# Performance work log

Hardware: AMD Instinct MI355X
Metric: run time of the kernel (lower is better)

The kernel has to match this reference:

```python
import jax, jax.numpy as jnp
import numpy as np

T, B, D, H = 1024, 128, 512, 256

def _linear_params(k, out_dim, in_dim):
    kw, kb = jax.random.split(k)
    s = 1.0 / np.sqrt(in_dim)
    w = jax.random.uniform(kw, (out_dim, in_dim), minval=-s, maxval=s, dtype=jnp.float32)
    b = jax.random.uniform(kb, (out_dim,), minval=-s, maxval=s, dtype=jnp.float32)
    return w, b

def setup_inputs() -> dict:
    key = jax.random.key(0)
    ks = jax.random.split(key, 9)
    x = jax.random.normal(ks[0], (T, B, D), dtype=jnp.float32)
    fc_w, fc_b = _linear_params(ks[1], H, D)
    forget_w, forget_b = _linear_params(ks[2], H, 2 * H)
    input_w, input_b = _linear_params(ks[3], H, 2 * H)
    update_w, update_b = _linear_params(ks[4], H, 2 * H)
    output_w, output_b = _linear_params(ks[5], H, 2 * H)
    cls_w0, cls_b0 = _linear_params(ks[6], H, H)
    cls_w1, cls_b1 = _linear_params(ks[7], H, H)
    cls_w2, cls_b2 = _linear_params(ks[8], 2, H)
    return dict(x=x, fc_w=fc_w, fc_b=fc_b,
                forget_w=forget_w, forget_b=forget_b,
                input_w=input_w, input_b=input_b,
                update_w=update_w, update_b=update_b,
                output_w=output_w, output_b=output_b,
                cls_w0=cls_w0, cls_b0=cls_b0,
                cls_w1=cls_w1, cls_b1=cls_b1,
                cls_w2=cls_w2, cls_b2=cls_b2)

def reference(x, fc_w, fc_b, forget_w, forget_b, input_w, input_b,
              update_w, update_b, output_w, output_b,
              cls_w0, cls_b0, cls_w1, cls_b1, cls_w2, cls_b2):
    # FC + tanh: [T,B,D] -> [T,B,H]
    h = jnp.tanh(x @ fc_w.T + fc_b)

    # LSTM-style gating over the leading time axis (state is [B,H])
    def step(carry, inp):
        hx, cx = carry
        comb = jnp.concatenate([inp, hx], axis=-1)  # [B, 2H]
        f = jax.nn.sigmoid(comb @ forget_w.T + forget_b)
        i = jax.nn.sigmoid(comb @ input_w.T + input_b)
        g = jnp.tanh(comb @ update_w.T + update_b)
        o = jax.nn.sigmoid(comb @ output_w.T + output_b)
        cx = f * cx + i * g
        hx = o * jnp.tanh(cx)
        return (hx, cx), hx

    init = (jnp.zeros((B, H), h.dtype), jnp.zeros((B, H), h.dtype))
    _, hs = jax.lax.scan(step, init, h)  # hs: [T,B,H]

    # classifier MLP (depth=2) -> 2 logits
    z = jax.nn.relu(hs @ cls_w0.T + cls_b0)
    z = jax.nn.relu(z @ cls_w1.T + cls_b1)
    return z @ cls_w2.T + cls_b2  # [T,B,2]
```

## Files before the change

kernel.cpp:

```cpp
#include <hip/hip_runtime.h>
#include <cstdint>

#define TT 1024
#define BB 128
#define DD 512
#define HH 256
#define TBR (TT*BB)

typedef __attribute__((ext_vector_type(8))) short  s8v;
typedef __attribute__((ext_vector_type(4))) float  f4v;
typedef __attribute__((ext_vector_type(4))) unsigned u4v;

__device__ __forceinline__ float sigf(float x) { return 1.0f / (1.0f + expf(-x)); }

__device__ __forceinline__ unsigned rnbf(float f) {
    unsigned u = __builtin_bit_cast(unsigned, f);
    return (u + 0x7FFFu + ((u >> 16) & 1u)) >> 16;
}

__global__ __launch_bounds__(256) void pack_kernel(
    const float* __restrict__ fw, const float* __restrict__ iw,
    const float* __restrict__ uw, const float* __restrict__ ow,
    const float* __restrict__ fb, const float* __restrict__ ib,
    const float* __restrict__ ub, const float* __restrict__ obb,
    float* __restrict__ wx_p, float* __restrict__ wh_p, float* __restrict__ b_p)
{
    const int r = blockIdx.x;
    const int gate = r >> 8, h = r & 255;
    const float* wsrc = gate == 0 ? fw : gate == 1 ? iw : gate == 2 ? uw : ow;
    const float* bsrc = gate == 0 ? fb : gate == 1 ? ib : gate == 2 ? ub : obb;
    const int k = threadIdx.x;
    wx_p[(size_t)r * 256 + k] = wsrc[(size_t)h * 512 + k];
    wh_p[(size_t)r * 256 + k] = wsrc[(size_t)h * 512 + 256 + k];
    if (k == 0) b_p[r] = bsrc[h];
}

__global__ __launch_bounds__(256) void pack_mfma(
    const float* __restrict__ fw, const float* __restrict__ iw,
    const float* __restrict__ uw, const float* __restrict__ ow,
    const float* __restrict__ fb, const float* __restrict__ ib,
    const float* __restrict__ ub, const float* __restrict__ obb,
    float* __restrict__ wx_p, float* __restrict__ wh_p, float* __restrict__ b_p)
{
    const int r = blockIdx.x;
    const int gate = (r >> 5) & 3;
    const int h = (r >> 7) * 32 + (r & 31);
    const float* wsrc = gate == 0 ? fw : gate == 1 ? iw : gate == 2 ? uw : ow;
    const float* bsrc = gate == 0 ? fb : gate == 1 ? ib : gate == 2 ? ub : obb;
    const int k = threadIdx.x;
    wx_p[(size_t)r * 256 + k] = wsrc[(size_t)h * 512 + k];
    wh_p[(size_t)r * 256 + k] = wsrc[(size_t)h * 512 + 256 + k];
    if (k == 0) b_p[r] = bsrc[h];
}

template<int K, int ACT, int PERM>
__global__ __launch_bounds__(256) void gemm_kernel(
    const float* A, const float* __restrict__ W,
    const float* __restrict__ bias, float* C, int N)
{
    __shared__ __align__(16) float As[16][192];
    __shared__ __align__(16) float Wt[16][192];
    const int tid = threadIdx.x;
    const int m0 = blockIdx.x * 128, n0 = blockIdx.y * 128;
    const int tm = tid >> 4, tn = tid & 15;
    const int am = tm * 12, wn = tn * 12;
    float acc[8][8] = {};
    for (int kc = 0; kc < K; kc += 16) {
        #pragma unroll
        for (int i = 0; i < 2; ++i) {
            int f4 = tid + 256 * i;
            int r = f4 >> 2, k4 = (f4 & 3) * 4;
            float4 av = *(const float4*)&A[(size_t)(m0 + r) * K + kc + k4];
            float4 wv = *(const float4*)&W[(size_t)(n0 + r) * K + kc + k4];
            int fo = (r >> 3) * 12 + (r & 7);
            As[k4 + 0][fo] = av.x; As[k4 + 1][fo] = av.y;
            As[k4 + 2][fo] = av.z; As[k4 + 3][fo] = av.w;
            Wt[k4 + 0][fo] = wv.x; Wt[k4 + 1][fo] = wv.y;
            Wt[k4 + 2][fo] = wv.z; Wt[k4 + 3][fo] = wv.w;
        }
        __syncthreads();
        #pragma unroll
        for (int kk = 0; kk < 16; ++kk) {
            float a[8], w[8];
            *(float4*)&a[0] = *(const float4*)&As[kk][am];
            *(float4*)&a[4] = *(const float4*)&As[kk][am + 4];
            *(float4*)&w[0] = *(const float4*)&Wt[kk][wn];
            *(float4*)&w[4] = *(const float4*)&Wt[kk][wn + 4];
            #pragma unroll
            for (int i = 0; i < 8; ++i)
                #pragma unroll
                for (int j = 0; j < 8; ++j)
                    acc[i][j] = fmaf(a[i], w[j], acc[i][j]);
        }
        __syncthreads();
    }
    #pragma unroll
    for (int i = 0; i < 8; ++i) {
        int m = m0 + tm * 8 + i;
        #pragma unroll
        for (int jh = 0; jh < 2; ++jh) {
            float4 v; float* vp = (float*)&v;
            #pragma unroll
            for (int l = 0; l < 4; ++l) {
                int n = n0 + tn * 8 + jh * 4 + l;
                float t = acc[i][jh * 4 + l] + bias[n];
                if (ACT == 1) t = tanhf(t);
                if (ACT == 2) t = fmaxf(t, 0.0f);
                vp[l] = t;
            }
            int nb = n0 + tn * 8 + jh * 4;
            int nc = PERM ? (((nb & 255) >> 3) * 32 + ((nb >> 8) << 3) + (nb & 7)) : nb;
            *(float4*)&C[(size_t)m * N + nc] = v;
        }
    }
}

__global__ __launch_bounds__(256, 1) void recur_mfma(
    float* __restrict__ h_buf,
    const float* __restrict__ xg,
    const float* __restrict__ wh_mf,
    unsigned* hxh, unsigned* hxl,
    int* flags)
{
    __shared__ __align__(16) unsigned ldsH[16 * 128];
    __shared__ __align__(16) unsigned ldsL[16 * 128];
    __shared__ float pre[16][132];
    const int tid = threadIdx.x;
    const int lane = tid & 63;
    const int wv = tid >> 6;
    const int bg = blockIdx.x & 7, hg = blockIdx.x >> 3;
    const int b0 = bg * 16;
    const int nlo = lane & 15, quad = lane >> 4;

    s8v bh[2][8], bl[2][8];
    #pragma unroll
    for (int nt = 0; nt < 2; ++nt) {
        int r = hg * 128 + wv * 32 + nt * 16 + nlo;
        #pragma unroll
        for (int ks = 0; ks < 8; ++ks) {
            const float* src = wh_mf + (size_t)r * 256 + ks * 32 + quad * 8;
            u4v uh, ul;
            #pragma unroll
            for (int p = 0; p < 4; ++p) {
                float f0 = src[2 * p], f1 = src[2 * p + 1];
                unsigned h0 = rnbf(f0), h1 = rnbf(f1);
                float r0 = f0 - __builtin_bit_cast(float, h0 << 16);
                float r1 = f1 - __builtin_bit_cast(float, h1 << 16);
                uh[p] = h0 | (rnbf(0.0f), h1 << 16);
                uh[p] = h0 | (h1 << 16);
                ul[p] = rnbf(r0) | (rnbf(r1) << 16);
            }
            bh[nt][ks] = __builtin_bit_cast(s8v, uh);
            bl[nt][ks] = __builtin_bit_cast(s8v, ul);
        }
    }

    const int sm = tid >> 4;
    const int sc0 = (tid & 15) * 2;
    const int cb = tid >> 4, q = tid & 15;

    float cx0 = 0.0f, cx1 = 0.0f;

    for (int t = 0; t < TT; ++t) {
        float2 xq[4];
        {
            const float* xr = xg + ((size_t)t * BB + b0 + cb) * 1024 + hg * 128 + 2 * q;
            #pragma unroll
            for (int g = 0; g < 4; ++g)
                xq[g] = *(const float2*)&xr[g * 32];
        }
        if (t > 0) {
            const int* fp = flags + ((size_t)(t - 1) * 8 + bg) * 8 + (lane & 7);
            long bud = 1L << 22;
            for (;;) {
                int v = __hip_atomic_load(fp, __ATOMIC_RELAXED, __HIP_MEMORY_SCOPE_AGENT);
                if (__all(v != 0)) break;
                if (--bud < 0) break;
                __builtin_amdgcn_s_sleep(1);
            }
        }
        {
            const size_t rowd = ((size_t)(t & 1) * 128 + b0 + sm) * 128 + sc0 * 4;
            const unsigned long long* gh = (const unsigned long long*)(hxh + rowd);
            const unsigned long long* gl = (const unsigned long long*)(hxl + rowd);
            unsigned long long a0 = __hip_atomic_load(gh + 0, __ATOMIC_RELAXED, __HIP_MEMORY_SCOPE_AGENT);
            unsigned long long a1 = __hip_atomic_load(gh + 1, __ATOMIC_RELAXED, __HIP_MEMORY_SCOPE_AGENT);
            unsigned long long a2 = __hip_atomic_load(gh + 2, __ATOMIC_RELAXED, __HIP_MEMORY_SCOPE_AGENT);
            unsigned long long a3 = __hip_atomic_load(gh + 3, __ATOMIC_RELAXED, __HIP_MEMORY_SCOPE_AGENT);
            unsigned long long c0 = __hip_atomic_load(gl + 0, __ATOMIC_RELAXED, __HIP_MEMORY_SCOPE_AGENT);
            unsigned long long c1 = __hip_atomic_load(gl + 1, __ATOMIC_RELAXED, __HIP_MEMORY_SCOPE_AGENT);
            unsigned long long c2 = __hip_atomic_load(gl + 2, __ATOMIC_RELAXED, __HIP_MEMORY_SCOPE_AGENT);
            unsigned long long c3 = __hip_atomic_load(gl + 3, __ATOMIC_RELAXED, __HIP_MEMORY_SCOPE_AGENT);
            int p0 = sm * 128 + ((sc0 ^ (sm & 7)) << 2);
            int p1 = sm * 128 + (((sc0 + 1) ^ (sm & 7)) << 2);
            u4v w0 = { (unsigned)a0, (unsigned)(a0 >> 32), (unsigned)a1, (unsigned)(a1 >> 32) };
            u4v w1 = { (unsigned)a2, (unsigned)(a2 >> 32), (unsigned)a3, (unsigned)(a3 >> 32) };
            u4v v0 = { (unsigned)c0, (unsigned)(c0 >> 32), (unsigned)c1, (unsigned)(c1 >> 32) };
            u4v v1 = { (unsigned)c2, (unsigned)(c2 >> 32), (unsigned)c3, (unsigned)(c3 >> 32) };
            *(u4v*)&ldsH[p0] = w0; *(u4v*)&ldsH[p1] = w1;
            *(u4v*)&ldsL[p0] = v0; *(u4v*)&ldsL[p1] = v1;
        }
        __syncthreads();

        f4v acc0 = {0.f, 0.f, 0.f, 0.f}, acc1 = {0.f, 0.f, 0.f, 0.f};
        #pragma unroll
        for (int ks = 0; ks < 8; ++ks) {
            int off = nlo * 128 + ((((ks * 4 + quad) ^ (nlo & 7))) << 2);
            s8v ah = __builtin_bit_cast(s8v, *(const u4v*)&ldsH[off]);
            s8v al = __builtin_bit_cast(s8v, *(const u4v*)&ldsL[off]);
            acc0 = __builtin_amdgcn_mfma_f32_16x16x32_bf16(ah, bh[0][ks], acc0, 0, 0, 0);
            acc1 = __builtin_amdgcn_mfma_f32_16x16x32_bf16(ah, bh[1][ks], acc1, 0, 0, 0);
            acc0 = __builtin_amdgcn_mfma_f32_16x16x32_bf16(al, bh[0][ks], acc0, 0, 0, 0);
            acc1 = __builtin_amdgcn_mfma_f32_16x16x32_bf16(al, bh[1][ks], acc1, 0, 0, 0);
            acc0 = __builtin_amdgcn_mfma_f32_16x16x32_bf16(ah, bl[0][ks], acc0, 0, 0, 0);
            acc1 = __builtin_amdgcn_mfma_f32_16x16x32_bf16(ah, bl[1][ks], acc1, 0, 0, 0);
        }
        {
            int n0c = wv * 32 + nlo;
            #pragma unroll
            for (int reg = 0; reg < 4; ++reg) {
                pre[quad * 4 + reg][n0c]      = acc0[reg];
                pre[quad * 4 + reg][n0c + 16] = acc1[reg];
            }
        }
        __syncthreads();

        float2 pf = *(const float2*)&pre[cb][0 * 32 + 2 * q];
        float2 pi = *(const float2*)&pre[cb][1 * 32 + 2 * q];
        float2 pg = *(const float2*)&pre[cb][2 * 32 + 2 * q];
        float2 po = *(const float2*)&pre[cb][3 * 32 + 2 * q];
        float f0 = sigf(pf.x + xq[0].x), f1 = sigf(pf.y + xq[0].y);
        float i0 = sigf(pi.x + xq[1].x), i1 = sigf(pi.y + xq[1].y);
        float g0 = tanhf(pg.x + xq[2].x), g1 = tanhf(pg.y + xq[2].y);
        float o0 = sigf(po.x + xq[3].x), o1 = sigf(po.y + xq[3].y);
        cx0 = f0 * cx0 + i0 * g0;
        cx1 = f1 * cx1 + i1 * g1;
        float hv0 = o0 * tanhf(cx0);
        float hv1 = o1 * tanhf(cx1);

        unsigned hb0 = rnbf(hv0), hb1 = rnbf(hv1);
        float l0 = hv0 - __builtin_bit_cast(float, hb0 << 16);
        float l1 = hv1 - __builtin_bit_cast(float, hb1 << 16);
        const size_t oc = ((size_t)((t + 1) & 1) * 128 + b0 + cb) * 128 + hg * 16 + q;
        __hip_atomic_store(&hxh[oc], hb0 | (hb1 << 16),
                           __ATOMIC_RELAXED, __HIP_MEMORY_SCOPE_AGENT);
        __hip_atomic_store(&hxl[oc], rnbf(l0) | (rnbf(l1) << 16),
                           __ATOMIC_RELAXED, __HIP_MEMORY_SCOPE_AGENT);
        *(float2*)&h_buf[((size_t)t * BB + b0 + cb) * 256 + hg * 32 + 2 * q] =
            make_float2(hv0, hv1);
        asm volatile("s_waitcnt vmcnt(0)" ::: "memory");
        __syncthreads();
        if (tid == 0)
            __hip_atomic_store(&flags[((size_t)t * 8 + bg) * 8 + hg], 1,
                               __ATOMIC_RELAXED, __HIP_MEMORY_SCOPE_AGENT);
    }
}

__device__ __forceinline__ int swz(int row, int k4) {
    return row * 256 + (((k4 ^ (row & 7)) & 63) << 2);
}

__global__ __launch_bounds__(256, 1) void recur_kernel(
    float* h_buf, const float* __restrict__ xg,
    const float* __restrict__ wx_p, const float* __restrict__ wh_p,
    const float* __restrict__ b_p, float* hx_buf, int* flags, int use_xg)
{
    __shared__ __align__(16) float Ws[32 * 256];
    __shared__ __align__(16) float Ss[32 * 256];
    const int tid = threadIdx.x;
    const int lane = tid & 63;
    const int bg = blockIdx.x & 3, hg = blockIdx.x >> 2;
    const int b0 = bg * 32;
    const int b = tid >> 3, h = tid & 7;
    const int wrow = tid >> 3;
    const int wkb = (tid & 7) * 32;

    float bias0 = b_p[0 * 256 + hg * 8 + h];
    float bias1 = b_p[1 * 256 + hg * 8 + h];
    float bias2 = b_p[2 * 256 + hg * 8 + h];
    float bias3 = b_p[3 * 256 + hg * 8 + h];
    __syncthreads();

    float cx = 0.0f, pv = 0.0f;

    for (int t = 0; t < TT; ++t) {
        if (t > 0) {
            const int* fp = flags + (size_t)(t - 1) * 128 + bg * 32 + (lane & 31);
            long bud = 1L << 22;
            for (;;) {
                int v = __hip_atomic_load(fp, __ATOMIC_RELAXED, __HIP_MEMORY_SCOPE_AGENT);
                if (__all(v != 0)) break;
                if (--bud < 0) break;
                __builtin_amdgcn_s_sleep(1);
            }
        }
        float acc0, acc1, acc2, acc3;
        {
            if (t > 0)
                h_buf[((size_t)(t - 1) * BB + b0 + b) * 256 + hg * 8 + h] = pv;
            acc0 = bias0; acc1 = bias1; acc2 = bias2; acc3 = bias3;
            {
                const int R = (wrow >> 3) * 256 + hg * 8 + (wrow & 7);
                const float* src = wx_p + (size_t)R * 256 + wkb;
                #pragma unroll
                for (int j = 0; j < 8; ++j)
                    *(float4*)&Ws[swz(wrow, (wkb >> 2) + j)] = *(const float4*)&src[j * 4];
                const float* hs = h_buf + ((size_t)t * BB + b0) * HH;
                #pragma unroll
                for (int i = 0; i < 32; ++i)
                    Ss[i * 256 + ((((tid >> 2) ^ (i & 7)) & 63) << 2) + (tid & 3)] =
                        hs[i * 256 + tid];
            }
            __syncthreads();
            #pragma unroll 4
            for (int k4 = 0; k4 < 64; ++k4) {
                float4 s  = *(const float4*)&Ss[swz(b, k4)];
                float4 w0 = *(const float4*)&Ws[(0 * 8 + h) * 256 + (((k4 ^ h) & 63) << 2)];
                float4 w1 = *(const float4*)&Ws[(1 * 8 + h) * 256 + (((k4 ^ h) & 63) << 2)];
                float4 w2 = *(const float4*)&Ws[(2 * 8 + h) * 256 + (((k4 ^ h) & 63) << 2)];
                float4 w3 = *(const float4*)&Ws[(3 * 8 + h) * 256 + (((k4 ^ h) & 63) << 2)];
                acc0 += s.x*w0.x + s.y*w0.y + s.z*w0.z + s.w*w0.w;
                acc1 += s.x*w1.x + s.y*w1.y + s.z*w1.z + s.w*w1.w;
                acc2 += s.x*w2.x + s.y*w2.y + s.z*w2.z + s.w*w2.w;
                acc3 += s.x*w3.x + s.y*w3.y + s.z*w3.z + s.w*w3.w;
            }
            __syncthreads();
            {
                const int R = (wrow >> 3) * 256 + hg * 8 + (wrow & 7);
                const float* src = wh_p + (size_t)R * 256 + wkb;
                #pragma unroll
                for (int j = 0; j < 8; ++j)
                    *(float4*)&Ws[swz(wrow, (wkb >> 2) + j)] = *(const float4*)&src[j * 4];
            }
        }
        {
            const float* hxr = hx_buf + (size_t)(t & 1) * (BB * HH) + (size_t)b0 * HH;
            #pragma unroll
            for (int i = 0; i < 32; ++i) {
                float v = __hip_atomic_load(&hxr[i * 256 + tid],
                                            __ATOMIC_RELAXED, __HIP_MEMORY_SCOPE_AGENT);
                Ss[i * 256 + ((((tid >> 2) ^ (i & 7)) & 63) << 2) + (tid & 3)] = v;
            }
        }
        __syncthreads();
        #pragma unroll 4
        for (int k4 = 0; k4 < 64; ++k4) {
            float4 s  = *(const float4*)&Ss[swz(b, k4)];
            float4 w0 = *(const float4*)&Ws[(0 * 8 + h) * 256 + (((k4 ^ h) & 63) << 2)];
            float4 w1 = *(const float4*)&Ws[(1 * 8 + h) * 256 + (((k4 ^ h) & 63) << 2)];
            float4 w2 = *(const float4*)&Ws[(2 * 8 + h) * 256 + (((k4 ^ h) & 63) << 2)];
            float4 w3 = *(const float4*)&Ws[(3 * 8 + h) * 256 + (((k4 ^ h) & 63) << 2)];
            acc0 += s.x*w0.x + s.y*w0.y + s.z*w0.z + s.w*w0.w;
            acc1 += s.x*w1.x + s.y*w1.y + s.z*w1.z + s.w*w1.w;
            acc2 += s.x*w2.x + s.y*w2.y + s.z*w2.z + s.w*w2.w;
            acc3 += s.x*w3.x + s.y*w3.y + s.z*w3.z + s.w*w3.w;
        }
        __syncthreads();

        float fg = sigf(acc0), ig = sigf(acc1), gg = tanhf(acc2), og = sigf(acc3);
        cx = fg * cx + ig * gg;
        float hxv = og * tanhf(cx);
        pv = hxv;

        __hip_atomic_store(
            &hx_buf[(size_t)((t + 1) & 1) * (BB * HH) + (size_t)(b0 + b) * HH + hg * 8 + h],
            hxv, __ATOMIC_RELAXED, __HIP_MEMORY_SCOPE_AGENT);
        asm volatile("s_waitcnt vmcnt(0)" ::: "memory");
        __syncthreads();
        if (tid == 0)
            __hip_atomic_store(&flags[(size_t)t * 128 + bg * 32 + hg], 1,
                               __ATOMIC_RELAXED, __HIP_MEMORY_SCOPE_AGENT);
    }

    {
        const int* fp = flags + (size_t)1023 * 128 + bg * 32 + (lane & 31);
        long bud = 1L << 22;
        for (;;) {
            int v = __hip_atomic_load(fp, __ATOMIC_RELAXED, __HIP_MEMORY_SCOPE_AGENT);
            if (__all(v != 0)) break;
            if (--bud < 0) break;
            __builtin_amdgcn_s_sleep(1);
        }
        h_buf[((size_t)1023 * BB + b0 + b) * 256 + hg * 8 + h] = pv;
    }
}

__global__ __launch_bounds__(256) void final_kernel(
    const float* __restrict__ z, const float* __restrict__ w2,
    const float* __restrict__ b2, float* __restrict__ out)
{
    const int m = blockIdx.x * 128 + (threadIdx.x >> 1);
    const int c = threadIdx.x & 1;
    const float* zr = z + (size_t)m * 256;
    const float* wr = w2 + (size_t)c * 256;
    float s = b2[c];
    #pragma unroll 8
    for (int k = 0; k < 256; k += 4) {
        float4 zv = *(const float4*)&zr[k];
        float4 wv = *(const float4*)&wr[k];
        s += zv.x*wv.x + zv.y*wv.y + zv.z*wv.z + zv.w*wv.w;
    }
    out[(size_t)m * 2 + c] = s;
}

extern "C" void kernel_launch(void* const* d_in, const int* in_sizes, int n_in,
                              void* d_out, int out_size, void* d_ws, size_t ws_size,
                              hipStream_t stream) {
    const float* x    = (const float*)d_in[0];
    const float* fc_w = (const float*)d_in[1];
    const float* fc_b = (const float*)d_in[2];
    const float* fw   = (const float*)d_in[3];
    const float* fb   = (const float*)d_in[4];
    const float* iw   = (const float*)d_in[5];
    const float* ib   = (const float*)d_in[6];
    const float* uw   = (const float*)d_in[7];
    const float* ub   = (const float*)d_in[8];
    const float* ow   = (const float*)d_in[9];
    const float* ob   = (const float*)d_in[10];
    const float* w0   = (const float*)d_in[11];
    const float* b0   = (const float*)d_in[12];
    const float* w1   = (const float*)d_in[13];
    const float* b1   = (const float*)d_in[14];
    const float* w2   = (const float*)d_in[15];
    const float* b2   = (const float*)d_in[16];
    float* out = (float*)d_out;

    float* ws = (float*)d_ws;
    size_t off = 0;
    float* h_buf  = ws + off; off += (size_t)TBR * HH;
    float* wx_p   = ws + off; off += 1024 * 256;
    float* wh_p   = ws + off; off += 1024 * 256;
    float* b_p    = ws + off; off += 1024;
    float* hx_buf = ws + off; off += 2 * BB * HH;
    float* sync_f = ws + off; off += 131072;
    const size_t base_f = off;
    float* xg = ws + base_f;
    const size_t need_xg = (base_f + (size_t)TBR * 1024) * sizeof(float);
    const int use_xg = (ws_size >= need_xg) ? 1 : 0;
    float* z0 = use_xg ? xg : (ws + base_f);

    unsigned* hxh   = (unsigned*)sync_f;
    unsigned* hxl   = hxh + 32768;
    int* flags_mf   = (int*)(hxl + 32768);
    int* flags_old  = (int*)sync_f;

    hipMemsetAsync(hx_buf, 0, (2 * BB * HH + 131072) * sizeof(float), stream);

    if (use_xg) {
        pack_mfma<<<1024, 256, 0, stream>>>(fw, iw, uw, ow, fb, ib, ub, ob,
                                            wx_p, wh_p, b_p);
        gemm_kernel<512, 1, 0><<<dim3(TBR / 128, 2), 256, 0, stream>>>(
            x, fc_w, fc_b, h_buf, 256);
        gemm_kernel<256, 0, 0><<<dim3(TBR / 128, 8), 256, 0, stream>>>(
            h_buf, wx_p, b_p, xg, 1024);
        recur_mfma<<<64, 256, 0, stream>>>(h_buf, xg, wh_p, hxh, hxl, flags_mf);
    } else {
        pack_kernel<<<1024, 256, 0, stream>>>(fw, iw, uw, ow, fb, ib, ub, ob,
                                              wx_p, wh_p, b_p);
        gemm_kernel<512, 1, 0><<<dim3(TBR / 128, 2), 256, 0, stream>>>(
            x, fc_w, fc_b, h_buf, 256);
        recur_kernel<<<128, 256, 0, stream>>>(h_buf, nullptr, wx_p, wh_p, b_p,
                                              hx_buf, flags_old, 0);
    }
    gemm_kernel<256, 2, 0><<<dim3(TBR / 128, 2), 256, 0, stream>>>(
        h_buf, w0, b0, z0, 256);
    gemm_kernel<256, 2, 0><<<dim3(TBR / 128, 2), 256, 0, stream>>>(
        z0, w1, b1, h_buf, 256);
    final_kernel<<<TBR / 128, 256, 0, stream>>>(h_buf, w2, b2, out);
}
```

Baseline: 4.997 ms.

## Replace flag barrier with sentinel-tagged 4-slot ring and fast activations

The recurrent kernel no longer publishes a per-step completion flag after a waitcnt and block barrier. Each thread now writes its hi/lo bf16 hidden pair as one 64-bit word into a 4-deep ring initialised to an all-ones sentinel. Consumers spin until none of their words equal the sentinel, and they reset the slot two steps back, which cuts one barrier, one fence and a flag round trip from the serial per-step critical path. Sigmoid and tanh also switch to fast exp and reciprocal approximations, which trades a small amount of accuracy. Correctness now depends on the sentinel never matching a real value and on ordering across the slot-reset and write steps.

```diff
diff --git a/kernel.cpp b/kernel.cpp
--- a/kernel.cpp
+++ b/kernel.cpp
@@ -11,7 +11,14 @@
 typedef __attribute__((ext_vector_type(4))) float  f4v;
 typedef __attribute__((ext_vector_type(4))) unsigned u4v;
 
-__device__ __forceinline__ float sigf(float x) { return 1.0f / (1.0f + expf(-x)); }
+__device__ __forceinline__ float sigf(float x) {
+    return __builtin_amdgcn_rcpf(1.0f + __expf(-x));
+}
+__device__ __forceinline__ float tanh_fast(float x) {
+    float e = __expf(fabsf(x) * 2.0f);
+    float t = 1.0f - 2.0f * __builtin_amdgcn_rcpf(e + 1.0f);
+    return copysignf(t, x);
+}
 
 __device__ __forceinline__ unsigned rnbf(float f) {
     unsigned u = __builtin_bit_cast(unsigned, f);
@@ -119,8 +126,7 @@
     float* __restrict__ h_buf,
     const float* __restrict__ xg,
     const float* __restrict__ wh_mf,
-    unsigned* hxh, unsigned* hxl,
-    int* flags)
+    unsigned long long* __restrict__ ring)
 {
     __shared__ __align__(16) unsigned ldsH[16 * 128];
     __shared__ __align__(16) unsigned ldsL[16 * 128];
@@ -146,7 +152,6 @@
                 unsigned h0 = rnbf(f0), h1 = rnbf(f1);
                 float r0 = f0 - __builtin_bit_cast(float, h0 << 16);
                 float r1 = f1 - __builtin_bit_cast(float, h1 << 16);
-                uh[p] = h0 | (rnbf(0.0f), h1 << 16);
                 uh[p] = h0 | (h1 << 16);
                 ul[p] = rnbf(r0) | (rnbf(r1) << 16);
             }
@@ -158,6 +163,7 @@
     const int sm = tid >> 4;
     const int sc0 = (tid & 15) * 2;
     const int cb = tid >> 4, q = tid & 15;
+    const unsigned long long SENT = ~0ull;
 
     float cx0 = 0.0f, cx1 = 0.0f;
 
@@ -169,36 +175,45 @@
             for (int g = 0; g < 4; ++g)
                 xq[g] = *(const float2*)&xr[g * 32];
         }
-        if (t > 0) {
-            const int* fp = flags + ((size_t)(t - 1) * 8 + bg) * 8 + (lane & 7);
+
+        const int p0 = sm * 128 + ((sc0 ^ (sm & 7)) << 2);
+        const int p1 = sm * 128 + (((sc0 + 1) ^ (sm & 7)) << 2);
+
+        if (t == 0) {
+            u4v z = {0u, 0u, 0u, 0u};
+            *(u4v*)&ldsH[p0] = z; *(u4v*)&ldsH[p1] = z;
+            *(u4v*)&ldsL[p0] = z; *(u4v*)&ldsL[p1] = z;
+        } else {
+            unsigned long long* src =
+                ring + ((size_t)((t - 1) & 3) * 128 + b0 + sm) * 128 + sc0 * 4;
+            unsigned long long a[8];
             long bud = 1L << 22;
             for (;;) {
-                int v = __hip_atomic_load(fp, __ATOMIC_RELAXED, __HIP_MEMORY_SCOPE_AGENT);
-                if (__all(v != 0)) break;
+                #pragma unroll
+                for (int i = 0; i < 8; ++i)
+                    a[i] = __hip_atomic_load(&src[i], __ATOMIC_RELAXED,
+                                             __HIP_MEMORY_SCOPE_AGENT);
+                bool ok = true;
+                #pragma unroll
+                for (int i = 0; i < 8; ++i) ok = ok && (a[i] != SENT);
+                if (__all(ok)) break;
                 if (--bud < 0) break;
                 __builtin_amdgcn_s_sleep(1);
             }
-        }
-        {
-            const size_t rowd = ((size_t)(t & 1) * 128 + b0 + sm) * 128 + sc0 * 4;
-            const unsigned long long* gh = (const unsigned long long*)(hxh + rowd);
-            const unsigned long long* gl = (const unsigned long long*)(hxl + rowd);
-            unsigned long long a0 = __hip_atomic_load(gh + 0, __ATOMIC_RELAXED, __HIP_MEMORY_SCOPE_AGENT);
-            unsigned long long a1 = __hip_atomic_load(gh + 1, __ATOMIC_RELAXED, __HIP_MEMORY_SCOPE_AGENT);
-            unsigned long long a2 = __hip_atomic_load(gh + 2, __ATOMIC_RELAXED, __HIP_MEMORY_SCOPE_AGENT);
-            unsigned long long a3 = __hip_atomic_load(gh + 3, __ATOMIC_RELAXED, __HIP_MEMORY_SCOPE_AGENT);
-            unsigned long long c0 = __hip_atomic_load(gl + 0, __ATOMIC_RELAXED, __HIP_MEMORY_SCOPE_AGENT);
-            unsigned long long c1 = __hip_atomic_load(gl + 1, __ATOMIC_RELAXED, __HIP_MEMORY_SCOPE_AGENT);
-            unsigned long long c2 = __hip_atomic_load(gl + 2, __ATOMIC_RELAXED, __HIP_MEMORY_SCOPE_AGENT);
-            unsigned long long c3 = __hip_atomic_load(gl + 3, __ATOMIC_RELAXED, __HIP_MEMORY_SCOPE_AGENT);
-            int p0 = sm * 128 + ((sc0 ^ (sm & 7)) << 2);
-            int p1 = sm * 128 + (((sc0 + 1) ^ (sm & 7)) << 2);
-            u4v w0 = { (unsigned)a0, (unsigned)(a0 >> 32), (unsigned)a1, (unsigned)(a1 >> 32) };
-            u4v w1 = { (unsigned)a2, (unsigned)(a2 >> 32), (unsigned)a3, (unsigned)(a3 >> 32) };
-            u4v v0 = { (unsigned)c0, (unsigned)(c0 >> 32), (unsigned)c1, (unsigned)(c1 >> 32) };
-            u4v v1 = { (unsigned)c2, (unsigned)(c2 >> 32), (unsigned)c3, (unsigned)(c3 >> 32) };
+            u4v w0 = { (unsigned)a[0], (unsigned)a[1], (unsigned)a[2], (unsigned)a[3] };
+            u4v w1 = { (unsigned)a[4], (unsigned)a[5], (unsigned)a[6], (unsigned)a[7] };
+            u4v v0 = { (unsigned)(a[0] >> 32), (unsigned)(a[1] >> 32),
+                       (unsigned)(a[2] >> 32), (unsigned)(a[3] >> 32) };
+            u4v v1 = { (unsigned)(a[4] >> 32), (unsigned)(a[5] >> 32),
+                       (unsigned)(a[6] >> 32), (unsigned)(a[7] >> 32) };
             *(u4v*)&ldsH[p0] = w0; *(u4v*)&ldsH[p1] = w1;
             *(u4v*)&ldsL[p0] = v0; *(u4v*)&ldsL[p1] = v1;
+
+            if (t >= 2) {
+                __hip_atomic_store(
+                    &ring[((size_t)((t - 2) & 3) * 128 + b0 + cb) * 128 + hg * 16 + q],
+                    SENT, __ATOMIC_RELAXED, __HIP_MEMORY_SCOPE_AGENT);
+            }
         }
         __syncthreads();
 
@@ -231,28 +246,24 @@
         float2 po = *(const float2*)&pre[cb][3 * 32 + 2 * q];
         float f0 = sigf(pf.x + xq[0].x), f1 = sigf(pf.y + xq[0].y);
         float i0 = sigf(pi.x + xq[1].x), i1 = sigf(pi.y + xq[1].y);
-        float g0 = tanhf(pg.x + xq[2].x), g1 = tanhf(pg.y + xq[2].y);
+        float g0 = tanh_fast(pg.x + xq[2].x), g1 = tanh_fast(pg.y + xq[2].y);
         float o0 = sigf(po.x + xq[3].x), o1 = sigf(po.y + xq[3].y);
         cx0 = f0 * cx0 + i0 * g0;
         cx1 = f1 * cx1 + i1 * g1;
-        float hv0 = o0 * tanhf(cx0);
-        float hv1 = o1 * tanhf(cx1);
+        float hv0 = o0 * tanh_fast(cx0);
+        float hv1 = o1 * tanh_fast(cx1);
 
         unsigned hb0 = rnbf(hv0), hb1 = rnbf(hv1);
         float l0 = hv0 - __builtin_bit_cast(float, hb0 << 16);
         float l1 = hv1 - __builtin_bit_cast(float, hb1 << 16);
-        const size_t oc = ((size_t)((t + 1) & 1) * 128 + b0 + cb) * 128 + hg * 16 + q;
-        __hip_atomic_store(&hxh[oc], hb0 | (hb1 << 16),
-                           __ATOMIC_RELAXED, __HIP_MEMORY_SCOPE_AGENT);
-        __hip_atomic_store(&hxl[oc], rnbf(l0) | (rnbf(l1) << 16),
-                           __ATOMIC_RELAXED, __HIP_MEMORY_SCOPE_AGENT);
+        unsigned long long atom =
+            (unsigned long long)(hb0 | (hb1 << 16)) |
+            ((unsigned long long)(rnbf(l0) | (rnbf(l1) << 16)) << 32);
+        __hip_atomic_store(
+            &ring[((size_t)(t & 3) * 128 + b0 + cb) * 128 + hg * 16 + q],
+            atom, __ATOMIC_RELAXED, __HIP_MEMORY_SCOPE_AGENT);
         *(float2*)&h_buf[((size_t)t * BB + b0 + cb) * 256 + hg * 32 + 2 * q] =
             make_float2(hv0, hv1);
-        asm volatile("s_waitcnt vmcnt(0)" ::: "memory");
-        __syncthreads();
-        if (tid == 0)
-            __hip_atomic_store(&flags[((size_t)t * 8 + bg) * 8 + hg], 1,
-                               __ATOMIC_RELAXED, __HIP_MEMORY_SCOPE_AGENT);
     }
 }
 
@@ -439,28 +450,24 @@
     const int use_xg = (ws_size >= need_xg) ? 1 : 0;
     float* z0 = use_xg ? xg : (ws + base_f);
 
-    unsigned* hxh   = (unsigned*)sync_f;
-    unsigned* hxl   = hxh + 32768;
-    int* flags_mf   = (int*)(hxl + 32768);
-    int* flags_old  = (int*)sync_f;
-
-    hipMemsetAsync(hx_buf, 0, (2 * BB * HH + 131072) * sizeof(float), stream);
-
     if (use_xg) {
+        hipMemsetAsync(sync_f, 0xFF, 131072 * sizeof(float), stream);
         pack_mfma<<<1024, 256, 0, stream>>>(fw, iw, uw, ow, fb, ib, ub, ob,
                                             wx_p, wh_p, b_p);
         gemm_kernel<512, 1, 0><<<dim3(TBR / 128, 2), 256, 0, stream>>>(
             x, fc_w, fc_b, h_buf, 256);
         gemm_kernel<256, 0, 0><<<dim3(TBR / 128, 8), 256, 0, stream>>>(
             h_buf, wx_p, b_p, xg, 1024);
-        recur_mfma<<<64, 256, 0, stream>>>(h_buf, xg, wh_p, hxh, hxl, flags_mf);
+        recur_mfma<<<64, 256, 0, stream>>>(h_buf, xg, wh_p,
+                                           (unsigned long long*)sync_f);
     } else {
+        hipMemsetAsync(hx_buf, 0, (2 * BB * HH + 131072) * sizeof(float), stream);
         pack_kernel<<<1024, 256, 0, stream>>>(fw, iw, uw, ow, fb, ib, ub, ob,
                                               wx_p, wh_p, b_p);
         gemm_kernel<512, 1, 0><<<dim3(TBR / 128, 2), 256, 0, stream>>>(
             x, fc_w, fc_b, h_buf, 256);
         recur_kernel<<<128, 256, 0, stream>>>(h_buf, nullptr, wx_p, wh_p, b_p,
-                                              hx_buf, flags_old, 0);
+                                              hx_buf, (int*)sync_f, 0);
     }
     gemm_kernel<256, 2, 0><<<dim3(TBR / 128, 2), 256, 0, stream>>>(
         h_buf, w0, b0, z0, 256);
```

Measured after the change: 4.687 ms. 1.07x faster.
